# Optimization experiments

Measured on AMD Instinct MI355X. Metric: run time of the kernel, lower is better.

Reference implementation:

```python
import jax, jax.numpy as jnp
import numpy as np

MARGIN = 0.5

def setup_inputs() -> dict:
    key = jax.random.key(0)
    k1, k2 = jax.random.split(key)
    inputs = jax.random.normal(k1, (8192, 256), dtype=jnp.float32)
    target = jax.random.randint(k2, (8192,), 0, 100, dtype=jnp.int64)
    return {"inputs": inputs, "target": target}

def reference(inputs, target):
    N = inputs.shape[0]
    # pairwise squared distances via ||xi||^2 + ||xj||^2 - 2 xi.xj
    sq = jnp.sum(inputs * inputs, axis=1)  # [N]
    gram = inputs @ inputs.T               # [N, N]
    distance = sq[:, None] + sq[None, :] - 2.0 * gram  # [N, N]
    R = (target[None, :] == target[:, None]).astype(inputs.dtype)  # [N, N]
    loss = R * distance + (1.0 - R) * jnp.maximum(MARGIN - distance, 0.0)
    return jnp.sum(loss) / (N * (N - 1.0) * 2.0)
```

## Files before the change

### kernel.cpp

```cpp
#include <hip/hip_runtime.h>
#include <stdint.h>

#define N     8192
#define KDIM  256
#define BM    128
#define BK    64
#define MARGIN 0.5f

typedef __bf16 bf16x8 __attribute__((ext_vector_type(8)));
typedef float  f32x4  __attribute__((ext_vector_type(4)));

__device__ __forceinline__ unsigned short f2bf(float f) {
    unsigned u = __float_as_uint(f);
    unsigned r = u + 0x7fffu + ((u >> 16) & 1u);
    return (unsigned short)(r >> 16);
}
__device__ __forceinline__ float bf2f(unsigned short s) {
    return __uint_as_float(((unsigned)s) << 16);
}

__device__ __forceinline__ void async_copy16(const void* g, void* l) {
    __builtin_amdgcn_global_load_lds(
        (__attribute__((address_space(1))) void*)(g),
        (__attribute__((address_space(3))) void*)(l),
        16, 0, 0);
}

__global__ __launch_bounds__(256) void prep_kernel(
        const float* __restrict__ X, unsigned short* __restrict__ Xb,
        float* __restrict__ sq) {
    int row  = blockIdx.x * 4 + (threadIdx.x >> 6);
    int lane = threadIdx.x & 63;

    const float4* src = (const float4*)(X + (size_t)row * KDIM) + lane;
    float4 v = *src;

    ushort4 o;
    o.x = f2bf(v.x); o.y = f2bf(v.y); o.z = f2bf(v.z); o.w = f2bf(v.w);
    float a = bf2f(o.x), b = bf2f(o.y), c = bf2f(o.z), d = bf2f(o.w);
    float ss = a * a + b * b + c * c + d * d;

    *((ushort4*)(Xb + (size_t)row * KDIM) + lane) = o;

    #pragma unroll
    for (int off = 32; off > 0; off >>= 1) ss += __shfl_down(ss, off, 64);
    if (lane == 0) sq[row] = ss;
}

__global__ __launch_bounds__(256) void loss_kernel(
        const unsigned short* __restrict__ Xb, const float* __restrict__ sq,
        const int* __restrict__ tgt, float* __restrict__ partials) {
    const int bj = blockIdx.x;
    const int bi = blockIdx.y;
    const int linear = bi * 64 + bj;

    if (bj < bi) {
        if (threadIdx.x == 0) partials[linear] = 0.0f;
        return;
    }

    __shared__ __align__(16) unsigned short As[BM * BK];
    __shared__ __align__(16) unsigned short Bs[BM * BK];
    __shared__ float sqa_s[BM], sqb_s[BM];
    __shared__ int   ta_s[BM],  tb_s[BM];
    __shared__ float wsum[4];

    const int tid  = threadIdx.x;
    const int wave = tid >> 6;
    const int lane = tid & 63;

    if (tid < 128) {
        sqa_s[tid] = sq[bi * BM + tid];
        ta_s[tid]  = tgt[bi * BM + tid];
    } else {
        int r = tid - 128;
        sqb_s[r] = sq[bj * BM + r];
        tb_s[r]  = tgt[bj * BM + r];
    }

    const int frow  = lane & 15;
    const int fquad = lane >> 4;

    f32x4 acc[4][4];
    #pragma unroll
    for (int im = 0; im < 4; ++im)
        #pragma unroll
        for (int in = 0; in < 4; ++in)
            acc[im][in] = (f32x4){0.f, 0.f, 0.f, 0.f};

    const int wm = (wave >> 1) * 64;
    const int wn = (wave & 1) * 64;

    const size_t rowA0 = (size_t)bi * BM;
    const size_t rowB0 = (size_t)bj * BM;

    const int lr = lane >> 3;
    const int cg = (lane & 7) ^ lr;

    for (int kt = 0; kt < KDIM / BK; ++kt) {
        const int k0 = kt * BK;
        #pragma unroll
        for (int q = 0; q < 4; ++q) {
            const int r0 = (wave * 4 + q) * 8;
            const unsigned short* gA =
                Xb + (rowA0 + r0 + lr) * KDIM + k0 + cg * 8;
            async_copy16(gA, (char*)As + r0 * 128);
            const unsigned short* gB =
                Xb + (rowB0 + r0 + lr) * KDIM + k0 + cg * 8;
            async_copy16(gB, (char*)Bs + r0 * 128);
        }
        __syncthreads();

        #pragma unroll
        for (int s = 0; s < 2; ++s) {
            const int gi = s * 4 + fquad;
            bf16x8 af[4], bfr[4];
            #pragma unroll
            for (int im = 0; im < 4; ++im) {
                int m = wm + im * 16 + frow;
                af[im] = *(const bf16x8*)((const char*)As +
                          m * 128 + ((gi ^ (m & 7)) * 16));
            }
            #pragma unroll
            for (int in = 0; in < 4; ++in) {
                int n = wn + in * 16 + frow;
                bfr[in] = *(const bf16x8*)((const char*)Bs +
                           n * 128 + ((gi ^ (n & 7)) * 16));
            }
            #pragma unroll
            for (int im = 0; im < 4; ++im)
                #pragma unroll
                for (int in = 0; in < 4; ++in)
                    acc[im][in] = __builtin_amdgcn_mfma_f32_16x16x32_bf16(
                        af[im], bfr[in], acc[im][in], 0, 0, 0);
        }
        __syncthreads();
    }

    float lsum = 0.0f;
    const bool diag = (bi == bj);
    #pragma unroll
    for (int im = 0; im < 4; ++im) {
        #pragma unroll
        for (int in = 0; in < 4; ++in) {
            #pragma unroll
            for (int r = 0; r < 4; ++r) {
                int rl = wm + im * 16 + fquad * 4 + r;
                int cl = wn + in * 16 + frow;
                float g = acc[im][in][r];
                float d = sqa_s[rl] + sqb_s[cl] - 2.0f * g;
                float c = (ta_s[rl] == tb_s[cl]) ? d
                                                 : fmaxf(MARGIN - d, 0.0f);
                float w = 2.0f;
                if (diag) w = (rl < cl) ? 2.0f : ((rl == cl) ? 1.0f : 0.0f);
                lsum += w * c;
            }
        }
    }

    #pragma unroll
    for (int off = 32; off > 0; off >>= 1) lsum += __shfl_down(lsum, off, 64);
    if (lane == 0) wsum[wave] = lsum;
    __syncthreads();
    if (tid == 0) partials[linear] = wsum[0] + wsum[1] + wsum[2] + wsum[3];
}

__global__ __launch_bounds__(256) void reduce_kernel(
        const float* __restrict__ partials, float* __restrict__ out,
        int n, float scale) {
    float s = 0.0f;
    for (int i = threadIdx.x; i < n; i += 256) s += partials[i];
    __shared__ float w[4];
    #pragma unroll
    for (int off = 32; off > 0; off >>= 1) s += __shfl_down(s, off, 64);
    int wave = threadIdx.x >> 6, lane = threadIdx.x & 63;
    if (lane == 0) w[wave] = s;
    __syncthreads();
    if (threadIdx.x == 0) out[0] = (w[0] + w[1] + w[2] + w[3]) * scale;
}

extern "C" void kernel_launch(void* const* d_in, const int* in_sizes, int n_in,
                              void* d_out, int out_size, void* d_ws, size_t ws_size,
                              hipStream_t stream) {
    (void)in_sizes; (void)n_in; (void)out_size; (void)ws_size;
    const float* X   = (const float*)d_in[0];
    const int*   tgt = (const int*)d_in[1];

    unsigned short* Xb = (unsigned short*)d_ws;
    float* sq       = (float*)((char*)d_ws + (size_t)N * KDIM * 2);
    float* partials = sq + N;

    prep_kernel<<<N / 4, 256, 0, stream>>>(X, Xb, sq);
    loss_kernel<<<dim3(64, 64), 256, 0, stream>>>(Xb, sq, tgt, partials);

    const float scale = (float)(1.0 / ((double)N * ((double)N - 1.0) * 2.0));
    reduce_kernel<<<1, 256, 0, stream>>>(partials, (float*)d_out, 64 * 64, scale);
}
```

Measured before the change: 97.14 us.

## Launch only upper-triangle tiles, stage full-K A tile in LDS, read B directly

The grid now covers only the upper-triangular tile pairs, found by inverting a triangular index with sqrt, so no blocks launch just to write a zero. The whole 128x256 A tile is loaded into LDS once with a single barrier, replacing the four K-step loop with two barriers each. B fragments are now read straight from global memory into registers instead of going through LDS, and the diagonal weighting is split into a separate branch. The risk is uncoalesced global B loads and a larger LDS footprint (64KB) that may lower occupancy.

```diff
diff --git a/kernel.cpp b/kernel.cpp
--- a/kernel.cpp
+++ b/kernel.cpp
@@ -1,10 +1,11 @@
 #include <hip/hip_runtime.h>
 #include <stdint.h>
 
-#define N     8192
-#define KDIM  256
-#define BM    128
-#define BK    64
+#define N      8192
+#define KDIM   256
+#define BM     128
+#define TILES  (N / BM)
+#define NPAIRS (TILES * (TILES + 1) / 2)
 #define MARGIN 0.5f
 
 typedef __bf16 bf16x8 __attribute__((ext_vector_type(8)));
@@ -32,14 +33,11 @@
     int row  = blockIdx.x * 4 + (threadIdx.x >> 6);
     int lane = threadIdx.x & 63;
 
-    const float4* src = (const float4*)(X + (size_t)row * KDIM) + lane;
-    float4 v = *src;
-
+    float4 v = *((const float4*)(X + (size_t)row * KDIM) + lane);
     ushort4 o;
     o.x = f2bf(v.x); o.y = f2bf(v.y); o.z = f2bf(v.z); o.w = f2bf(v.w);
     float a = bf2f(o.x), b = bf2f(o.y), c = bf2f(o.z), d = bf2f(o.w);
     float ss = a * a + b * b + c * c + d * d;
-
     *((ushort4*)(Xb + (size_t)row * KDIM) + lane) = o;
 
     #pragma unroll
@@ -50,17 +48,15 @@
 __global__ __launch_bounds__(256) void loss_kernel(
         const unsigned short* __restrict__ Xb, const float* __restrict__ sq,
         const int* __restrict__ tgt, float* __restrict__ partials) {
-    const int bj = blockIdx.x;
-    const int bi = blockIdx.y;
-    const int linear = bi * 64 + bj;
-
-    if (bj < bi) {
-        if (threadIdx.x == 0) partials[linear] = 0.0f;
-        return;
-    }
-
-    __shared__ __align__(16) unsigned short As[BM * BK];
-    __shared__ __align__(16) unsigned short Bs[BM * BK];
+    const int p = blockIdx.x;
+    float tf = 2.0f * TILES + 1.0f;
+    int bi = (int)((tf - sqrtf(tf * tf - 8.0f * (float)p)) * 0.5f);
+    if (bi < 0) bi = 0;
+    while (bi > 0 && (bi * TILES - bi * (bi - 1) / 2) > p) --bi;
+    while (((bi + 1) * TILES - (bi + 1) * bi / 2) <= p) ++bi;
+    const int bj = bi + (p - (bi * TILES - bi * (bi - 1) / 2));
+
+    __shared__ __align__(16) unsigned short As[BM * KDIM];
     __shared__ float sqa_s[BM], sqb_s[BM];
     __shared__ int   ta_s[BM],  tb_s[BM];
     __shared__ float wsum[4];
@@ -78,9 +74,28 @@
         tb_s[r]  = tgt[bj * BM + r];
     }
 
+    const size_t rowA0 = (size_t)bi * BM;
+    const size_t rowB0 = (size_t)bj * BM;
+
+    {
+        const int lr32 = lane >> 5;
+        const int slot = lane & 31;
+        const int rw   = wave * 2 + lr32;
+        const int g0   = slot ^ rw;
+        const unsigned short* gA = Xb + (rowA0 + rw) * KDIM + g0 * 8;
+        char* ldst = (char*)As + wave * 2 * 512;
+        #pragma unroll
+        for (int i = 0; i < 16; ++i)
+            async_copy16(gA + (size_t)i * 8 * KDIM, ldst + i * 4096);
+    }
+    __syncthreads();
+
     const int frow  = lane & 15;
     const int fquad = lane >> 4;
 
+    const int wm = (wave >> 1) * 64;
+    const int wn = (wave & 1) * 64;
+
     f32x4 acc[4][4];
     #pragma unroll
     for (int im = 0; im < 4; ++im)
@@ -88,72 +103,66 @@
         for (int in = 0; in < 4; ++in)
             acc[im][in] = (f32x4){0.f, 0.f, 0.f, 0.f};
 
-    const int wm = (wave >> 1) * 64;
-    const int wn = (wave & 1) * 64;
-
-    const size_t rowA0 = (size_t)bi * BM;
-    const size_t rowB0 = (size_t)bj * BM;
-
-    const int lr = lane >> 3;
-    const int cg = (lane & 7) ^ lr;
-
-    for (int kt = 0; kt < KDIM / BK; ++kt) {
-        const int k0 = kt * BK;
-        #pragma unroll
-        for (int q = 0; q < 4; ++q) {
-            const int r0 = (wave * 4 + q) * 8;
-            const unsigned short* gA =
-                Xb + (rowA0 + r0 + lr) * KDIM + k0 + cg * 8;
-            async_copy16(gA, (char*)As + r0 * 128);
-            const unsigned short* gB =
-                Xb + (rowB0 + r0 + lr) * KDIM + k0 + cg * 8;
-            async_copy16(gB, (char*)Bs + r0 * 128);
-        }
-        __syncthreads();
-
-        #pragma unroll
-        for (int s = 0; s < 2; ++s) {
-            const int gi = s * 4 + fquad;
-            bf16x8 af[4], bfr[4];
+    const unsigned short* bptr[4];
+    #pragma unroll
+    for (int in = 0; in < 4; ++in)
+        bptr[in] = Xb + (rowB0 + wn + in * 16 + frow) * KDIM + fquad * 8;
+
+    const char* abase = (const char*)As + (wm + frow) * 512;
+    const int   fr7   = frow & 7;
+
+    #pragma unroll
+    for (int ks = 0; ks < 8; ++ks) {
+        const int slotA = ((ks * 4 + fquad) ^ fr7) << 4;
+        bf16x8 af[4], bfr[4];
+        #pragma unroll
+        for (int im = 0; im < 4; ++im)
+            af[im] = *(const bf16x8*)(abase + im * 16 * 512 + slotA);
+        #pragma unroll
+        for (int in = 0; in < 4; ++in)
+            bfr[in] = *(const bf16x8*)(bptr[in] + ks * 32);
+        #pragma unroll
+        for (int im = 0; im < 4; ++im)
             #pragma unroll
-            for (int im = 0; im < 4; ++im) {
-                int m = wm + im * 16 + frow;
-                af[im] = *(const bf16x8*)((const char*)As +
-                          m * 128 + ((gi ^ (m & 7)) * 16));
-            }
+            for (int in = 0; in < 4; ++in)
+                acc[im][in] = __builtin_amdgcn_mfma_f32_16x16x32_bf16(
+                    af[im], bfr[in], acc[im][in], 0, 0, 0);
+    }
+
+    float lsum = 0.0f;
+    if (bi != bj) {
+        #pragma unroll
+        for (int im = 0; im < 4; ++im) {
             #pragma unroll
             for (int in = 0; in < 4; ++in) {
-                int n = wn + in * 16 + frow;
-                bfr[in] = *(const bf16x8*)((const char*)Bs +
-                           n * 128 + ((gi ^ (n & 7)) * 16));
+                #pragma unroll
+                for (int r = 0; r < 4; ++r) {
+                    int rl = wm + im * 16 + fquad * 4 + r;
+                    int cl = wn + in * 16 + frow;
+                    float d = fmaf(-2.0f, acc[im][in][r],
+                                   sqa_s[rl] + sqb_s[cl]);
+                    lsum += (ta_s[rl] == tb_s[cl]) ? d
+                                                   : fmaxf(MARGIN - d, 0.0f);
+                }
             }
+        }
+        lsum *= 2.0f;
+    } else {
+        #pragma unroll
+        for (int im = 0; im < 4; ++im) {
             #pragma unroll
-            for (int im = 0; im < 4; ++im)
+            for (int in = 0; in < 4; ++in) {
                 #pragma unroll
-                for (int in = 0; in < 4; ++in)
-                    acc[im][in] = __builtin_amdgcn_mfma_f32_16x16x32_bf16(
-                        af[im], bfr[in], acc[im][in], 0, 0, 0);
-        }
-        __syncthreads();
-    }
-
-    float lsum = 0.0f;
-    const bool diag = (bi == bj);
-    #pragma unroll
-    for (int im = 0; im < 4; ++im) {
-        #pragma unroll
-        for (int in = 0; in < 4; ++in) {
-            #pragma unroll
-            for (int r = 0; r < 4; ++r) {
-                int rl = wm + im * 16 + fquad * 4 + r;
-                int cl = wn + in * 16 + frow;
-                float g = acc[im][in][r];
-                float d = sqa_s[rl] + sqb_s[cl] - 2.0f * g;
-                float c = (ta_s[rl] == tb_s[cl]) ? d
-                                                 : fmaxf(MARGIN - d, 0.0f);
-                float w = 2.0f;
-                if (diag) w = (rl < cl) ? 2.0f : ((rl == cl) ? 1.0f : 0.0f);
-                lsum += w * c;
+                for (int r = 0; r < 4; ++r) {
+                    int rl = wm + im * 16 + fquad * 4 + r;
+                    int cl = wn + in * 16 + frow;
+                    float d = fmaf(-2.0f, acc[im][in][r],
+                                   sqa_s[rl] + sqb_s[cl]);
+                    float c = (ta_s[rl] == tb_s[cl]) ? d
+                                                     : fmaxf(MARGIN - d, 0.0f);
+                    float w = (rl < cl) ? 2.0f : ((rl == cl) ? 1.0f : 0.0f);
+                    lsum += w * c;
+                }
             }
         }
     }
@@ -162,7 +171,7 @@
     for (int off = 32; off > 0; off >>= 1) lsum += __shfl_down(lsum, off, 64);
     if (lane == 0) wsum[wave] = lsum;
     __syncthreads();
-    if (tid == 0) partials[linear] = wsum[0] + wsum[1] + wsum[2] + wsum[3];
+    if (tid == 0) partials[p] = wsum[0] + wsum[1] + wsum[2] + wsum[3];
 }
 
 __global__ __launch_bounds__(256) void reduce_kernel(
@@ -191,8 +200,8 @@
     float* partials = sq + N;
 
     prep_kernel<<<N / 4, 256, 0, stream>>>(X, Xb, sq);
-    loss_kernel<<<dim3(64, 64), 256, 0, stream>>>(Xb, sq, tgt, partials);
+    loss_kernel<<<NPAIRS, 256, 0, stream>>>(Xb, sq, tgt, partials);
 
     const float scale = (float)(1.0 / ((double)N * ((double)N - 1.0) * 2.0));
-    reduce_kernel<<<1, 256, 0, stream>>>(partials, (float*)d_out, 64 * 64, scale);
-}
+    reduce_kernel<<<1, 256, 0, stream>>>(partials, (float*)d_out, NPAIRS, scale);
+}
```

New measurement: 110.0 us. 1.13x slower.
